# Kernel optimization log

Measured on AMD Instinct MI355X. Metric: run time of the kernel, lower is better.

Reference implementation:

```python
import jax, jax.numpy as jnp
import numpy as np

N_NODES = 100000
N_EDGES = 1600000
D_IN = 128
D_OUT = 128


def setup_inputs() -> dict:
    key = jax.random.key(0)
    k_x, k_w, k_r, k_c, k_v = jax.random.split(key, 5)
    x = jax.random.normal(k_x, (N_NODES, D_IN), dtype=jnp.float32)
    # xavier_uniform: U(-a, a), a = sqrt(6/(fan_in+fan_out))
    a = float(np.sqrt(6.0 / (D_IN + D_OUT)))
    W = jax.random.uniform(k_w, (D_IN, D_OUT), dtype=jnp.float32, minval=-a, maxval=a)
    edge_row = jax.random.randint(k_r, (N_EDGES,), 0, N_NODES, dtype=jnp.int32)
    edge_col = jax.random.randint(k_c, (N_EDGES,), 0, N_NODES, dtype=jnp.int32)
    edge_val = jax.random.uniform(k_v, (N_EDGES,), dtype=jnp.float32)
    return {"x": x, "W": W, "edge_row": edge_row, "edge_col": edge_col, "edge_val": edge_val}


def reference(x, W, edge_row, edge_col, edge_val):
    # dropout with p=0.0 is the identity (module default), so omitted.
    support = x @ W                                  # [N, D_OUT] dense GEMM
    # sparse adj @ support in COO form: out[r] += v * support[c]
    msgs = support[edge_col] * edge_val[:, None]      # [E, D_OUT] irregular gather
    out = jax.ops.segment_sum(msgs, edge_row, num_segments=x.shape[0])
    return jnp.tanh(out)
```

## Files before the change

### kernel.cpp

```cpp
#include <hip/hip_runtime.h>
#include <hip/hip_bf16.h>
#include <hip/hip_fp16.h>
#include <math.h>

#define D 128
#define BIN_SHIFT 9
#define BIN_ROWS 512
#define NB_MAX 256
#define CPAD 16
#define AW 8192
#define NCB 16
#define CB_SHIFT 13
#define CKEYS (BIN_ROWS * NCB)

typedef _Float16 half8 __attribute__((ext_vector_type(8)));
typedef float floatx4 __attribute__((ext_vector_type(4)));
typedef float floatx2 __attribute__((ext_vector_type(2)));

__device__ __forceinline__ int cslot(int k) { return ((k & 31) << 8) | (k >> 5); }

__global__ void gcn_wt_kernel(const float* __restrict__ W,
                              unsigned short* __restrict__ wt,
                              int* __restrict__ cbin) {
    const int i = blockIdx.x * 256 + threadIdx.x;
    const int n = i >> 7, k = i & 127;
    wt[i] = __half_as_ushort(__float2half_rn(W[k * D + n]));
    if (blockIdx.x == 0) cbin[threadIdx.x] = 0;
}

__global__ __launch_bounds__(256) void gcn_gemm_kernel(
        const float* __restrict__ x, const unsigned short* __restrict__ wt,
        unsigned short* __restrict__ support2, int n_nodes) {
    const int wave = threadIdx.x >> 6;
    const int lane = threadIdx.x & 63;
    const int q = lane >> 4;
    const int n16 = lane & 15;
    const int row_base = blockIdx.x * 128 + wave * 32;
    if (row_base >= n_nodes) return;

    const half8* wt8 = (const half8*)wt;

    floatx4 acc[2][8];
#pragma unroll
    for (int mt = 0; mt < 2; ++mt)
#pragma unroll
        for (int nt = 0; nt < 8; ++nt) acc[mt][nt] = (floatx4){0.f, 0.f, 0.f, 0.f};

#pragma unroll
    for (int kc = 0; kc < 4; ++kc) {
        half8 b[8];
#pragma unroll
        for (int nt = 0; nt < 8; ++nt)
            b[nt] = wt8[(nt * 16 + n16) * 16 + kc * 4 + q];
#pragma unroll
        for (int mt = 0; mt < 2; ++mt) {
            const float* xp = x + (size_t)(row_base + mt * 16 + n16) * D
                                + kc * 32 + q * 8;
            const float4 f0 = *(const float4*)xp;
            const float4 f1 = *(const float4*)(xp + 4);
            half8 a;
            a[0] = (_Float16)f0.x; a[1] = (_Float16)f0.y;
            a[2] = (_Float16)f0.z; a[3] = (_Float16)f0.w;
            a[4] = (_Float16)f1.x; a[5] = (_Float16)f1.y;
            a[6] = (_Float16)f1.z; a[7] = (_Float16)f1.w;
#pragma unroll
            for (int nt = 0; nt < 8; ++nt)
                acc[mt][nt] = __builtin_amdgcn_mfma_f32_16x16x32_f16(
                    a, b[nt], acc[mt][nt], 0, 0, 0);
        }
    }

#pragma unroll
    for (int mt = 0; mt < 2; ++mt) {
        const int r0 = row_base + mt * 16 + q * 4;
#pragma unroll
        for (int nt = 0; nt < 8; ++nt) {
            const int col = nt * 16 + n16;
#pragma unroll
            for (int i = 0; i < 4; ++i)
                support2[(size_t)(r0 + i) * D + col] =
                    __half_as_ushort(__float2half_rn(acc[mt][nt][i]));
        }
    }
}

__global__ __launch_bounds__(256) void gcn_chist_kernel(
        const int* __restrict__ erow, int* __restrict__ cbin, int n_edges) {
    __shared__ int h[NB_MAX];
    const int t = threadIdx.x;
    h[t] = 0;
    __syncthreads();
    const int stride = gridDim.x * 256 * 4;
    const int nv = n_edges & ~3;
    for (int i = (blockIdx.x * 256 + t) * 4; i + 3 < n_edges; i += stride) {
        const int4 r = *(const int4*)(erow + i);
        atomicAdd(&h[r.x >> BIN_SHIFT], 1);
        atomicAdd(&h[r.y >> BIN_SHIFT], 1);
        atomicAdd(&h[r.z >> BIN_SHIFT], 1);
        atomicAdd(&h[r.w >> BIN_SHIFT], 1);
    }
    if (blockIdx.x == 0) {
        for (int i = nv + t; i < n_edges; i += 256)
            atomicAdd(&h[erow[i] >> BIN_SHIFT], 1);
    }
    __syncthreads();
    if (h[t] > 0) atomicAdd(&cbin[t], h[t]);
}

__global__ void gcn_cscan_kernel(const int* __restrict__ cbin,
                                 int* __restrict__ cbase,
                                 int* __restrict__ ccur,
                                 int* __restrict__ offsets,
                                 int nbins, int n_nodes, int n_edges) {
    __shared__ int sm[256];
    const int t = threadIdx.x;
    const int v = (t < nbins) ? cbin[t] : 0;
    sm[t] = v;
    __syncthreads();
    for (int off = 1; off < 256; off <<= 1) {
        int tv = (t >= off) ? sm[t - off] : 0;
        __syncthreads();
        sm[t] += tv;
        __syncthreads();
    }
    const int ex = sm[t] - v;
    if (t < nbins) { cbase[t] = ex; ccur[t * CPAD] = ex; }
    if (t == 0) { cbase[nbins] = n_edges; offsets[n_nodes] = n_edges; }
}

__global__ __launch_bounds__(256) void gcn_binA_kernel(
        const int* __restrict__ erow, const int* __restrict__ ecol,
        const float* __restrict__ eval, int* __restrict__ ccur,
        uint2* __restrict__ tmp8, int n_edges, int nbins) {
    __shared__ uint2 recs[AW];
    __shared__ int hist[NB_MAX];
    __shared__ int lstart[NB_MAX];
    __shared__ int gbase[NB_MAX];
    const int t = threadIdx.x;
    const int w0 = blockIdx.x * AW;
    const int wend = min(w0 + AW, n_edges);
    const int cnt = wend - w0;

    for (int i = t; i < NB_MAX; i += 256) hist[i] = 0;
    __syncthreads();

    for (int i = w0 + t; i < wend; i += 256)
        atomicAdd(&hist[erow[i] >> BIN_SHIFT], 1);
    __syncthreads();

    {
        const int v = hist[t];
        gbase[t] = v;
        __syncthreads();
        for (int off = 1; off < 256; off <<= 1) {
            int tv = (t >= off) ? gbase[t - off] : 0;
            __syncthreads();
            gbase[t] += tv;
            __syncthreads();
        }
        lstart[t] = gbase[t] - v;
        __syncthreads();
    }

    {
        const int c = hist[t];
        int gb = 0;
        if (t < nbins && c > 0) gb = atomicAdd(&ccur[t * CPAD], c);
        __syncthreads();
        gbase[t] = gb;
        hist[t] = lstart[t];
    }
    __syncthreads();

    for (int i = w0 + t; i < wend; i += 256) {
        const int r = erow[i];
        const int c = ecol[i];
        const unsigned short vh = __half_as_ushort(__float2half_rn(eval[i]));
        const int b = r >> BIN_SHIFT;
        const int p = atomicAdd(&hist[b], 1);
        recs[p] = make_uint2(((unsigned)r << 15) | vh, (unsigned)c);
    }
    __syncthreads();

    for (int s = t; s < cnt; s += 256) {
        const uint2 rec = recs[s];
        const int b = (int)(rec.x >> 15) >> BIN_SHIFT;
        tmp8[gbase[b] + (s - lstart[b])] = rec;
    }
}

__global__ __launch_bounds__(256) void gcn_binB_kernel(
        const uint2* __restrict__ tmp8, const int* __restrict__ cbase,
        int* __restrict__ offsets,
        unsigned int* __restrict__ rec4, int n_nodes) {
    __shared__ int cnt[CKEYS];
    __shared__ int sm[256];
    const int bin = blockIdx.x;
    const int r0 = bin << BIN_SHIFT;
    const int t = threadIdx.x;
    for (int i = t; i < CKEYS; i += 256) cnt[i] = 0;
    __syncthreads();

    const int beg = cbase[bin];
    const int end = cbase[bin + 1];

    for (int i = beg + t; i < end; i += 256) {
        const uint2 p = tmp8[i];
        const int k = (((int)(p.x >> 15) - r0) << 4) | (int)(p.y >> CB_SHIFT);
        atomicAdd(&cnt[cslot(k)], 1);
    }
    __syncthreads();

    int sum = 0;
#pragma unroll
    for (int i = 0; i < 32; ++i) sum += cnt[(i << 8) | t];
    sm[t] = sum;
    __syncthreads();
    for (int off = 1; off < 256; off <<= 1) {
        int tv = (t >= off) ? sm[t - off] : 0;
        __syncthreads();
        sm[t] += tv;
        __syncthreads();
    }
    int run = sm[t] - sum;
#pragma unroll
    for (int i = 0; i < 32; ++i) {
        const int s = (i << 8) | t;
        const int c = cnt[s];
        cnt[s] = run;
        run += c;
    }
    __syncthreads();

    for (int lr = t; lr < BIN_ROWS; lr += 256) {
        const int row = r0 + lr;
        if (row < n_nodes) offsets[row] = beg + cnt[cslot(lr << 4)];
    }
    __syncthreads();

    for (int i = beg + t; i < end; i += 256) {
        const uint2 p = tmp8[i];
        const int k = (((int)(p.x >> 15) - r0) << 4) | (int)(p.y >> CB_SHIFT);
        const int pos = beg + atomicAdd(&cnt[cslot(k)], 1);
        rec4[pos] = (p.y << 15) | (p.x & 0x7FFFu);
    }
}

__global__ __launch_bounds__(256) void gcn_gather_kernel(
        const unsigned int* __restrict__ support_u,
        const unsigned int* __restrict__ rec4,
        const int* __restrict__ offsets,
        float* __restrict__ out, int n_nodes) {
    const int node = __builtin_amdgcn_readfirstlane(
        blockIdx.x * 4 + (threadIdx.x >> 6));
    const int lane = threadIdx.x & 63;
    if (node >= n_nodes) return;

    const int beg = offsets[node];
    const int end = offsets[node + 1];

    float ax = 0.f, ay = 0.f, bx = 0.f, by = 0.f;
    int e = beg;
    for (; e + 7 < end; e += 8) {
        unsigned r[8], s[8];
#pragma unroll
        for (int j = 0; j < 8; ++j) r[j] = rec4[e + j];
#pragma unroll
        for (int j = 0; j < 8; ++j)
            s[j] = support_u[(size_t)(r[j] >> 15) * 64 + lane];
#pragma unroll
        for (int j = 0; j < 8; ++j) {
            const float v = __half2float(__ushort_as_half((unsigned short)(r[j] & 0x7FFFu)));
            const float slo = __half2float(__ushort_as_half((unsigned short)(s[j] & 0xFFFFu)));
            const float shi = __half2float(__ushort_as_half((unsigned short)(s[j] >> 16)));
            if (j & 1) { bx += v * slo; by += v * shi; }
            else       { ax += v * slo; ay += v * shi; }
        }
    }
    for (; e + 3 < end; e += 4) {
        unsigned r[4], s[4];
#pragma unroll
        for (int j = 0; j < 4; ++j) r[j] = rec4[e + j];
#pragma unroll
        for (int j = 0; j < 4; ++j)
            s[j] = support_u[(size_t)(r[j] >> 15) * 64 + lane];
#pragma unroll
        for (int j = 0; j < 4; ++j) {
            const float v = __half2float(__ushort_as_half((unsigned short)(r[j] & 0x7FFFu)));
            const float slo = __half2float(__ushort_as_half((unsigned short)(s[j] & 0xFFFFu)));
            const float shi = __half2float(__ushort_as_half((unsigned short)(s[j] >> 16)));
            if (j & 1) { bx += v * slo; by += v * shi; }
            else       { ax += v * slo; ay += v * shi; }
        }
    }
    for (; e < end; ++e) {
        const unsigned r = rec4[e];
        const unsigned s = support_u[(size_t)(r >> 15) * 64 + lane];
        const float v = __half2float(__ushort_as_half((unsigned short)(r & 0x7FFFu)));
        ax += v * __half2float(__ushort_as_half((unsigned short)(s & 0xFFFFu)));
        ay += v * __half2float(__ushort_as_half((unsigned short)(s >> 16)));
    }

    floatx2 res;
    res.x = tanhf(ax + bx);
    res.y = tanhf(ay + by);
    floatx2* out2 = (floatx2*)out;
    __builtin_nontemporal_store(res, &out2[(size_t)node * 64 + lane]);
}

extern "C" void kernel_launch(void* const* d_in, const int* in_sizes, int n_in,
                              void* d_out, int out_size, void* d_ws, size_t ws_size,
                              hipStream_t stream) {
    const float* x    = (const float*)d_in[0];
    const float* W    = (const float*)d_in[1];
    const int*   erow = (const int*)d_in[2];
    const int*   ecol = (const int*)d_in[3];
    const float* eval = (const float*)d_in[4];
    float* out = (float*)d_out;

    const int n_nodes = in_sizes[0] / D;
    const int n_edges = in_sizes[2];
    const int nbins = (n_nodes + BIN_ROWS - 1) >> BIN_SHIFT;

    unsigned short* support2 = (unsigned short*)d_ws;
    unsigned short* wt = support2 + (size_t)n_nodes * D;
    uint2* tmp8   = (uint2*)(wt + D * D);
    unsigned int* rec4 = (unsigned int*)(tmp8 + n_edges);
    int*  offsets = (int*)(rec4 + n_edges);
    int*  cbin    = offsets + n_nodes + 1;
    int*  cbase   = cbin + NB_MAX;
    int*  ccur    = cbase + NB_MAX + 1;

    gcn_wt_kernel<<<(D * D) / 256, 256, 0, stream>>>(W, wt, cbin);
    gcn_gemm_kernel<<<(n_nodes + 127) / 128, 256, 0, stream>>>(
        x, wt, support2, n_nodes);

    gcn_chist_kernel<<<320, 256, 0, stream>>>(erow, cbin, n_edges);
    gcn_cscan_kernel<<<1, 256, 0, stream>>>(cbin, cbase, ccur, offsets,
                                            nbins, n_nodes, n_edges);

    gcn_binA_kernel<<<(n_edges + AW - 1) / AW, 256, 0, stream>>>(
        erow, ecol, eval, ccur, tmp8, n_edges, nbins);
    gcn_binB_kernel<<<nbins, 256, 0, stream>>>(tmp8, cbase, offsets, rec4, n_nodes);

    gcn_gather_kernel<<<(n_nodes + 3) / 4, 256, 0, stream>>>(
        (const unsigned int*)support2, rec4, offsets, out, n_nodes);
}
```

Measured before the change: 260.9 us.

## Use smaller row bins and drop column sub-bucketing in the edge sort

```diff
diff --git a/kernel.cpp b/kernel.cpp
--- a/kernel.cpp
+++ b/kernel.cpp
@@ -4,20 +4,15 @@
 #include <math.h>
 
 #define D 128
-#define BIN_SHIFT 9
-#define BIN_ROWS 512
-#define NB_MAX 256
+#define BIN_SHIFT 8
+#define BIN_ROWS 256
+#define NB_MAX 512
 #define CPAD 16
-#define AW 8192
-#define NCB 16
-#define CB_SHIFT 13
-#define CKEYS (BIN_ROWS * NCB)
+#define AW 4096
 
 typedef _Float16 half8 __attribute__((ext_vector_type(8)));
 typedef float floatx4 __attribute__((ext_vector_type(4)));
 typedef float floatx2 __attribute__((ext_vector_type(2)));
-
-__device__ __forceinline__ int cslot(int k) { return ((k & 31) << 8) | (k >> 5); }
 
 __global__ void gcn_wt_kernel(const float* __restrict__ W,
                               unsigned short* __restrict__ wt,
@@ -25,7 +20,7 @@
     const int i = blockIdx.x * 256 + threadIdx.x;
     const int n = i >> 7, k = i & 127;
     wt[i] = __half_as_ushort(__float2half_rn(W[k * D + n]));
-    if (blockIdx.x == 0) cbin[threadIdx.x] = 0;
+    if (blockIdx.x < 2) cbin[blockIdx.x * 256 + threadIdx.x] = 0;
 }
 
 __global__ __launch_bounds__(256) void gcn_gemm_kernel(
@@ -89,6 +84,7 @@
     __shared__ int h[NB_MAX];
     const int t = threadIdx.x;
     h[t] = 0;
+    h[t + 256] = 0;
     __syncthreads();
     const int stride = gridDim.x * 256 * 4;
     const int nv = n_edges & ~3;
@@ -105,19 +101,19 @@
     }
     __syncthreads();
     if (h[t] > 0) atomicAdd(&cbin[t], h[t]);
-}
-
-__global__ void gcn_cscan_kernel(const int* __restrict__ cbin,
-                                 int* __restrict__ cbase,
-                                 int* __restrict__ ccur,
-                                 int* __restrict__ offsets,
-                                 int nbins, int n_nodes, int n_edges) {
-    __shared__ int sm[256];
+    if (h[t + 256] > 0) atomicAdd(&cbin[t + 256], h[t + 256]);
+}
+
+__global__ __launch_bounds__(512) void gcn_cscan_kernel(
+        const int* __restrict__ cbin, int* __restrict__ cbase,
+        int* __restrict__ ccur, int* __restrict__ offsets,
+        int nbins, int n_nodes, int n_edges) {
+    __shared__ int sm[512];
     const int t = threadIdx.x;
     const int v = (t < nbins) ? cbin[t] : 0;
     sm[t] = v;
     __syncthreads();
-    for (int off = 1; off < 256; off <<= 1) {
+    for (int off = 1; off < 512; off <<= 1) {
         int tv = (t >= off) ? sm[t - off] : 0;
         __syncthreads();
         sm[t] += tv;
@@ -128,7 +124,7 @@
     if (t == 0) { cbase[nbins] = n_edges; offsets[n_nodes] = n_edges; }
 }
 
-__global__ __launch_bounds__(256) void gcn_binA_kernel(
+__global__ __launch_bounds__(512) void gcn_binA_kernel(
         const int* __restrict__ erow, const int* __restrict__ ecol,
         const float* __restrict__ eval, int* __restrict__ ccur,
         uint2* __restrict__ tmp8, int n_edges, int nbins) {
@@ -141,10 +137,10 @@
     const int wend = min(w0 + AW, n_edges);
     const int cnt = wend - w0;
 
-    for (int i = t; i < NB_MAX; i += 256) hist[i] = 0;
-    __syncthreads();
-
-    for (int i = w0 + t; i < wend; i += 256)
+    hist[t] = 0;
+    __syncthreads();
+
+    for (int i = w0 + t; i < wend; i += 512)
         atomicAdd(&hist[erow[i] >> BIN_SHIFT], 1);
     __syncthreads();
 
@@ -152,7 +148,7 @@
         const int v = hist[t];
         gbase[t] = v;
         __syncthreads();
-        for (int off = 1; off < 256; off <<= 1) {
+        for (int off = 1; off < 512; off <<= 1) {
             int tv = (t >= off) ? gbase[t - off] : 0;
             __syncthreads();
             gbase[t] += tv;
@@ -172,7 +168,7 @@
     }
     __syncthreads();
 
-    for (int i = w0 + t; i < wend; i += 256) {
+    for (int i = w0 + t; i < wend; i += 512) {
         const int r = erow[i];
         const int c = ecol[i];
         const unsigned short vh = __half_as_ushort(__float2half_rn(eval[i]));
@@ -182,7 +178,7 @@
     }
     __syncthreads();
 
-    for (int s = t; s < cnt; s += 256) {
+    for (int s = t; s < cnt; s += 512) {
         const uint2 rec = recs[s];
         const int b = (int)(rec.x >> 15) >> BIN_SHIFT;
         tmp8[gbase[b] + (s - lstart[b])] = rec;
@@ -193,55 +189,41 @@
         const uint2* __restrict__ tmp8, const int* __restrict__ cbase,
         int* __restrict__ offsets,
         unsigned int* __restrict__ rec4, int n_nodes) {
-    __shared__ int cnt[CKEYS];
-    __shared__ int sm[256];
+    __shared__ int cnt[BIN_ROWS];
+    __shared__ int sm[BIN_ROWS];
     const int bin = blockIdx.x;
     const int r0 = bin << BIN_SHIFT;
     const int t = threadIdx.x;
-    for (int i = t; i < CKEYS; i += 256) cnt[i] = 0;
+    cnt[t] = 0;
     __syncthreads();
 
     const int beg = cbase[bin];
     const int end = cbase[bin + 1];
 
+    for (int i = beg + t; i < end; i += 256)
+        atomicAdd(&cnt[(int)(tmp8[i].x >> 15) - r0], 1);
+    __syncthreads();
+
+    const int v = cnt[t];
+    sm[t] = v;
+    __syncthreads();
+    for (int off = 1; off < 256; off <<= 1) {
+        int tv = (t >= off) ? sm[t - off] : 0;
+        __syncthreads();
+        sm[t] += tv;
+        __syncthreads();
+    }
+    const int mypos = beg + sm[t] - v;
+
+    const int row = r0 + t;
+    if (row < n_nodes) offsets[row] = mypos;
+    __syncthreads();
+    cnt[t] = mypos;
+    __syncthreads();
+
     for (int i = beg + t; i < end; i += 256) {
         const uint2 p = tmp8[i];
-        const int k = (((int)(p.x >> 15) - r0) << 4) | (int)(p.y >> CB_SHIFT);
-        atomicAdd(&cnt[cslot(k)], 1);
-    }
-    __syncthreads();
-
-    int sum = 0;
-#pragma unroll
-    for (int i = 0; i < 32; ++i) sum += cnt[(i << 8) | t];
-    sm[t] = sum;
-    __syncthreads();
-    for (int off = 1; off < 256; off <<= 1) {
-        int tv = (t >= off) ? sm[t - off] : 0;
-        __syncthreads();
-        sm[t] += tv;
-        __syncthreads();
-    }
-    int run = sm[t] - sum;
-#pragma unroll
-    for (int i = 0; i < 32; ++i) {
-        const int s = (i << 8) | t;
-        const int c = cnt[s];
-        cnt[s] = run;
-        run += c;
-    }
-    __syncthreads();
-
-    for (int lr = t; lr < BIN_ROWS; lr += 256) {
-        const int row = r0 + lr;
-        if (row < n_nodes) offsets[row] = beg + cnt[cslot(lr << 4)];
-    }
-    __syncthreads();
-
-    for (int i = beg + t; i < end; i += 256) {
-        const uint2 p = tmp8[i];
-        const int k = (((int)(p.x >> 15) - r0) << 4) | (int)(p.y >> CB_SHIFT);
-        const int pos = beg + atomicAdd(&cnt[cslot(k)], 1);
+        const int pos = atomicAdd(&cnt[(int)(p.x >> 15) - r0], 1);
         rec4[pos] = (p.y << 15) | (p.x & 0x7FFFu);
     }
 }
@@ -336,10 +318,10 @@
         x, wt, support2, n_nodes);
 
     gcn_chist_kernel<<<320, 256, 0, stream>>>(erow, cbin, n_edges);
-    gcn_cscan_kernel<<<1, 256, 0, stream>>>(cbin, cbase, ccur, offsets,
+    gcn_cscan_kernel<<<1, 512, 0, stream>>>(cbin, cbase, ccur, offsets,
                                             nbins, n_nodes, n_edges);
 
-    gcn_binA_kernel<<<(n_edges + AW - 1) / AW, 256, 0, stream>>>(
+    gcn_binA_kernel<<<(n_edges + AW - 1) / AW, 512, 0, stream>>>(
         erow, ecol, eval, ccur, tmp8, n_edges, nbins);
     gcn_binB_kernel<<<nbins, 256, 0, stream>>>(tmp8, cbase, offsets, rec4, n_nodes);
 
```

Result: faster. 241.3 us (-7.5%).
